# Optimization experiments

Hardware: AMD Instinct MI355X
Metric: run time of the kernel (lower is better)

The kernel has to match this reference:

```python
import jax, jax.numpy as jnp
import numpy as np

B, S, E = 4, 2048, 1024
H, D = 16, 64  # num_heads, head_size; H*D == E


def setup_inputs() -> dict:
    key = jax.random.key(0)
    ks = jax.random.split(key, 6)
    scale = E ** -0.5
    x = jax.random.normal(ks[0], (B, S, E), dtype=jnp.float32)
    # per-head bias-free q/k/v projections, stacked over heads: [H, E, D]
    Wq = jax.random.normal(ks[1], (H, E, D), dtype=jnp.float32) * scale
    Wk = jax.random.normal(ks[2], (H, E, D), dtype=jnp.float32) * scale
    Wv = jax.random.normal(ks[3], (H, E, D), dtype=jnp.float32) * scale
    # output projection: Linear(H*D, E) with bias
    Wproj = jax.random.normal(ks[4], (H * D, E), dtype=jnp.float32) * ((H * D) ** -0.5)
    bproj = jax.random.normal(ks[5], (E,), dtype=jnp.float32) * 0.01
    return {"x": x, "Wq": Wq, "Wk": Wk, "Wv": Wv, "Wproj": Wproj, "bproj": bproj}


def reference(x, Wq, Wk, Wv, Wproj, bproj):
    # Batched equivalent of the per-head loop: each head h computes
    # q = x @ Wq[h], k = x @ Wk[h], v = x @ Wv[h]
    q = jnp.einsum("bse,hed->bhsd", x, Wq)
    k = jnp.einsum("bse,hed->bhsd", x, Wk)
    v = jnp.einsum("bse,hed->bhsd", x, Wv)
    # causal scaled dot-product attention, scale = head_size**-0.5
    scores = jnp.einsum("bhqd,bhkd->bhqk", q, k) * (D ** -0.5)
    causal = jnp.tril(jnp.ones((S, S), dtype=bool))  # [S, S]
    scores = jnp.where(causal, scores, jnp.finfo(scores.dtype).min)
    attn = jax.nn.softmax(scores, axis=-1)  # dropout = identity in eval
    out = jnp.einsum("bhqk,bhkd->bhqd", attn, v)
    # concat heads along the feature dim, then project (dropout = identity)
    out = out.transpose(0, 2, 1, 3).reshape(B, S, H * D)
    return out @ Wproj + bproj
```

## Files before the change

kernel.cpp:

```cpp
#include <hip/hip_runtime.h>
#include <stdint.h>

typedef unsigned short u16;
typedef __attribute__((ext_vector_type(8))) short bf16x8;
typedef __attribute__((ext_vector_type(8))) unsigned short u16x8;
typedef __attribute__((ext_vector_type(4))) float f32x4;

#define S_LEN 2048
#define EDIM 1024
#define NH 16
#define HD 64

static __device__ __forceinline__ u16 f2bf(float f) {
  union { float f; uint32_t u; } v; v.f = f;
  uint32_t r = v.u + 0x7fffu + ((v.u >> 16) & 1u);
  return (u16)(r >> 16);
}

static __device__ __forceinline__ uint32_t cvtpk_bf16(float a, float b) {
  uint32_t r;
  asm("v_cvt_pk_bf16_f32 %0, %1, %2" : "=v"(r) : "v"(a), "v"(b));
  return r;
}

static __device__ __forceinline__ void gload_lds16(const u16* g, u16* l) {
  __builtin_amdgcn_global_load_lds(
      (const __attribute__((address_space(1))) void*)g,
      (__attribute__((address_space(3))) void*)l, 16, 0, 0);
}

static __device__ __forceinline__ bf16x8 gload16(const u16* p) {
  bf16x8 r;
  asm volatile("global_load_dwordx4 %0, %1, off" : "=v"(r) : "v"(p));
  return r;
}

#define WAIT_VM(n)                                   \
  do {                                               \
    asm volatile("s_waitcnt vmcnt(" #n ")");         \
    __builtin_amdgcn_sched_barrier(0);               \
  } while (0)

#define BARRIER()                                    \
  do {                                               \
    __builtin_amdgcn_s_barrier();                    \
    __builtin_amdgcn_sched_barrier(0);               \
  } while (0)

__global__ __launch_bounds__(256) void pack_inputs(
    const float* __restrict__ x, const float* __restrict__ Wq,
    const float* __restrict__ Wk, const float* __restrict__ Wv,
    const float* __restrict__ Wp,
    u16* __restrict__ xb, u16* __restrict__ wqkvT, u16* __restrict__ wprojT) {
  const int blk = blockIdx.x;
  const int tid = threadIdx.x;
  if (blk < 8192) {
    int idx = blk * 256 + tid;
    float4 v = ((const float4*)x)[idx];
    ushort4 o;
    o.x = f2bf(v.x); o.y = f2bf(v.y); o.z = f2bf(v.z); o.w = f2bf(v.w);
    ((ushort4*)xb)[idx] = o;
    return;
  }
  __shared__ u16 tile[64][65];
  const float* src;
  size_t src_rs;
  u16* dst;
  float wscale = 1.0f;
  if (blk < 8960) {
    int t = blk - 8192;
    int mh = t >> 4;
    int et = t & 15;
    int m = mh >> 4, h = mh & 15;
    const float* W = (m == 0) ? Wq : (m == 1) ? Wk : Wv;
    if (m == 0) wscale = 0.1803368801111204f;
    src = W + ((size_t)(h * EDIM + et * 64)) * HD;
    src_rs = HD;
    dst = wqkvT + (size_t)(m * 1024 + h * 64) * 1024 + et * 64;
  } else {
    int t = blk - 8960;
    int kt = t >> 4, nt = t & 15;
    src = Wp + (size_t)(kt * 64) * 1024 + nt * 64;
    src_rs = 1024;
    dst = wprojT + (size_t)(nt * 64) * 1024 + kt * 64;
  }
  {
    const int rr = tid >> 4;
    const int c4 = (tid & 15) << 2;
#pragma unroll
    for (int p = 0; p < 4; p++) {
      const int r = p * 16 + rr;
      float4 v = *(const float4*)(src + (size_t)r * src_rs + c4);
      tile[r][c4 + 0] = f2bf(v.x * wscale);
      tile[r][c4 + 1] = f2bf(v.y * wscale);
      tile[r][c4 + 2] = f2bf(v.z * wscale);
      tile[r][c4 + 3] = f2bf(v.w * wscale);
    }
  }
  __syncthreads();
  {
    const int rr = tid >> 3;
    const int c8 = (tid & 7) << 3;
#pragma unroll
    for (int p = 0; p < 2; p++) {
      const int r = p * 32 + rr;
      u16x8 o;
#pragma unroll
      for (int j = 0; j < 8; j++) o[j] = tile[c8 + j][r];
      *(u16x8*)(dst + (size_t)r * 1024 + c8) = o;
    }
  }
}

template <int EPI>
__global__ __launch_bounds__(256) void gemm128(
    const u16* __restrict__ A, const u16* __restrict__ Bt,
    const float* __restrict__ bias,
    u16* __restrict__ o0, u16* __restrict__ o1, u16* __restrict__ o2,
    float* __restrict__ of, int K, int N) {
  __shared__ __align__(16) u16 As[128 * 64];
  __shared__ __align__(16) u16 Bs[128 * 64];
  const int tid  = threadIdx.x;
  const int lane = tid & 63;
  const int wave = tid >> 6;
  const int wm = wave >> 1;
  const int wn = wave & 1;
  const int col = lane & 15;
  const int quad = lane >> 4;
  const int cs = col & 7;
  const int m0 = blockIdx.y << 7;
  const int n0 = blockIdx.x << 7;

  const int srow  = lane >> 3;
  const int sslot = (lane & 7) ^ srow;
  const u16* gA = A + (size_t)(m0 + (wave << 5) + srow) * K + sslot * 8;
  const u16* gB = Bt + (size_t)(n0 + (wave << 5) + srow) * K + sslot * 8;
  u16* lA = &As[(wave << 5) << 6];
  u16* lB = &Bs[(wave << 5) << 6];

  f32x4 acc[4][4];
#pragma unroll
  for (int i = 0; i < 4; i++)
#pragma unroll
    for (int j = 0; j < 4; j++) acc[i][j] = (f32x4){0.f, 0.f, 0.f, 0.f};

  for (int kk = 0; kk < K; kk += 64) {
    __syncthreads();
#pragma unroll
    for (int i = 0; i < 4; i++) {
      gload_lds16(gA + (size_t)(i * 8) * K + kk, lA + i * 512);
      gload_lds16(gB + (size_t)(i * 8) * K + kk, lB + i * 512);
    }
    __syncthreads();

#pragma unroll
    for (int x = 0; x < 2; x++) {
      bf16x8 af[4], bfr[4];
#pragma unroll
      for (int i = 0; i < 4; i++)
        af[i] = *(const bf16x8*)(
            &As[((wm * 64 + i * 16 + col) << 6) + ((((x << 2) + quad) ^ cs) << 3)]);
#pragma unroll
      for (int j = 0; j < 4; j++)
        bfr[j] = *(const bf16x8*)(
            &Bs[((wn * 64 + j * 16 + col) << 6) + ((((x << 2) + quad) ^ cs) << 3)]);
#pragma unroll
      for (int i = 0; i < 4; i++)
#pragma unroll
        for (int j = 0; j < 4; j++)
          acc[i][j] = __builtin_amdgcn_mfma_f32_16x16x32_bf16(af[i], bfr[j],
                                                              acc[i][j], 0, 0, 0);
    }
  }

#pragma unroll
  for (int i = 0; i < 4; i++) {
#pragma unroll
    for (int j = 0; j < 4; j++) {
      const int rg0 = m0 + wm * 64 + i * 16 + quad * 4;
      const int cg = n0 + wn * 64 + j * 16 + col;
      if (EPI == 0) {
        const int mat = cg >> 10;
        const int rem = cg & 1023;
        const int h = rem >> 6;
        const int d = rem & 63;
        const int b = rg0 >> 11;
        const int s0 = rg0 & 2047;
        if (mat == 2) {
          ushort4 o;
          o.x = f2bf(acc[i][j][0]); o.y = f2bf(acc[i][j][1]);
          o.z = f2bf(acc[i][j][2]); o.w = f2bf(acc[i][j][3]);
          *(ushort4*)(&o2[(((size_t)(b * NH + h) * HD + d) << 11) + s0]) = o;
        } else {
          u16* dst = (mat == 0) ? o0 : o1;
#pragma unroll
          for (int r = 0; r < 4; r++)
            dst[((size_t)((b * NH + h) * S_LEN + s0 + r) << 6) + d] =
                f2bf(acc[i][j][r]);
        }
      } else {
#pragma unroll
        for (int r = 0; r < 4; r++)
          of[(size_t)(rg0 + r) * N + cg] = acc[i][j][r] + bias[cg];
      }
    }
  }
}

__global__ __launch_bounds__(512, 4) void attn_fused(
    const u16* __restrict__ Q, const u16* __restrict__ K,
    const u16* __restrict__ Vt, u16* __restrict__ O) {
  __shared__ __align__(16) u16 Kbuf[2][64 * 64];
  __shared__ __align__(16) u16 Vbuf[2][64 * 64];
  __shared__ __align__(16) u16 Ps[8][16 * 72];

  const int tid  = threadIdx.x;
  const int lane = tid & 63;
  const int wave = tid >> 6;
  const int col  = lane & 15;
  const int quad = lane >> 4;
  const int cs   = col & 7;
  const int gid  = blockIdx.x;
  const int bh = ((gid & 7) << 3) | ((gid >> 3) & 7);
  const int hi = gid >> 6;
  const int qb = (hi < 4) ? (7 - hi) : (hi - 4);
  const int b = bh >> 4;
  const int h = bh & 15;
  const int q0w = qb * 256 + wave * 32;

  const u16* Kbh = K + (size_t)bh * S_LEN * HD;
  const u16* Vbh = Vt + (size_t)bh * HD * S_LEN;

  const int srow  = lane >> 3;
  const int sslot = (lane & 7) ^ srow;
  const int r0 = wave * 8;

  bf16x8 qf[2][2];
#pragma unroll
  for (int a = 0; a < 2; a++) {
    const u16* Qrow = Q + ((size_t)bh * S_LEN + q0w + a * 16 + col) * HD;
    qf[a][0] = gload16(Qrow + quad * 8);
    qf[a][1] = gload16(Qrow + 32 + quad * 8);
  }

  f32x4 oacc[2][4];
#pragma unroll
  for (int a = 0; a < 2; a++)
#pragma unroll
    for (int n = 0; n < 4; n++) oacc[a][n] = (f32x4){0.f, 0.f, 0.f, 0.f};
  float lrow[2][4] = {{0.f, 0.f, 0.f, 0.f}, {0.f, 0.f, 0.f, 0.f}};

  auto STAGE = [&](int buf, int kv0) {
    gload_lds16(Kbh + (size_t)(kv0 + r0 + srow) * HD + sslot * 8,
                &Kbuf[buf][r0 * 64]);
    gload_lds16(Vbh + (size_t)(r0 + srow) * S_LEN + kv0 + sslot * 8,
                &Vbuf[buf][r0 * 64]);
  };

  const int T = 4 * qb + 4;
  int cur = 0;
  STAGE(0, 0);
  WAIT_VM(0);
  BARRIER();

  for (int t = 0; t < T; t++) {
    const int kv0 = t << 6;
    if (t + 1 < T) STAGE(cur ^ 1, kv0 + 64);

    if (kv0 <= q0w + 31) {
      f32x4 sc[2][4];
#pragma unroll
      for (int j = 0; j < 4; j++) {
        const u16* kr = &Kbuf[cur][(j * 16 + col) * 64];
        const bf16x8 kf0 = *(const bf16x8*)(kr + ((quad ^ cs) << 3));
        const bf16x8 kf1 = *(const bf16x8*)(kr + (((4 + quad) ^ cs) << 3));
#pragma unroll
        for (int a = 0; a < 2; a++) {
          sc[a][j] = (f32x4){0.f, 0.f, 0.f, 0.f};
          sc[a][j] = __builtin_amdgcn_mfma_f32_16x16x32_bf16(qf[a][0], kf0, sc[a][j], 0, 0, 0);
          sc[a][j] = __builtin_amdgcn_mfma_f32_16x16x32_bf16(qf[a][1], kf1, sc[a][j], 0, 0, 0);
        }
      }

      const bool diag = (kv0 + 63 > q0w);
#pragma unroll
      for (int a = 0; a < 2; a++) {
#pragma unroll
        for (int r = 0; r < 4; r++) {
          float p[4];
#pragma unroll
          for (int j = 0; j < 4; j++) {
            float v = exp2f(sc[a][j][r]);
            if (diag) {
              const int ql = q0w - kv0 + a * 16 + quad * 4 + r;
              if (j * 16 + col > ql) v = 0.f;
            }
            lrow[a][r] += v;
            p[j] = v;
          }
          const uint32_t pk0 = cvtpk_bf16(p[0], p[1]);
          const uint32_t pk1 = cvtpk_bf16(p[2], p[3]);
          u16* row = &Ps[wave][(quad * 4 + r) * 72 + col];
          row[0]  = (u16)pk0;
          row[16] = (u16)(pk0 >> 16);
          row[32] = (u16)pk1;
          row[48] = (u16)(pk1 >> 16);
        }
        const bf16x8 pf0 = *(const bf16x8*)(&Ps[wave][col * 72 + quad * 8]);
        const bf16x8 pf1 = *(const bf16x8*)(&Ps[wave][col * 72 + 32 + quad * 8]);
#pragma unroll
        for (int n = 0; n < 4; n++) {
          const u16* vr = &Vbuf[cur][(n * 16 + col) * 64];
          const bf16x8 vf0 = *(const bf16x8*)(vr + ((quad ^ cs) << 3));
          const bf16x8 vf1 = *(const bf16x8*)(vr + (((4 + quad) ^ cs) << 3));
          oacc[a][n] = __builtin_amdgcn_mfma_f32_16x16x32_bf16(pf0, vf0, oacc[a][n], 0, 0, 0);
          oacc[a][n] = __builtin_amdgcn_mfma_f32_16x16x32_bf16(pf1, vf1, oacc[a][n], 0, 0, 0);
        }
      }
    }

    WAIT_VM(0);
    BARRIER();
    cur ^= 1;
  }

#pragma unroll
  for (int a = 0; a < 2; a++)
#pragma unroll
    for (int r = 0; r < 4; r++) {
      float l = lrow[a][r];
#pragma unroll
      for (int off = 1; off < 16; off <<= 1) l += __shfl_xor(l, off);
      const float inv = 1.0f / l;
      const size_t row = (size_t)b * S_LEN + q0w + a * 16 + quad * 4 + r;
#pragma unroll
      for (int n = 0; n < 4; n++)
        O[row * EDIM + h * HD + n * 16 + col] = f2bf(oacc[a][n][r] * inv);
    }
}

extern "C" void kernel_launch(void* const* d_in, const int* in_sizes, int n_in,
                              void* d_out, int out_size, void* d_ws, size_t ws_size,
                              hipStream_t stream) {
  const float* x  = (const float*)d_in[0];
  const float* Wq = (const float*)d_in[1];
  const float* Wk = (const float*)d_in[2];
  const float* Wv = (const float*)d_in[3];
  const float* Wp = (const float*)d_in[4];
  const float* bp = (const float*)d_in[5];
  float* out = (float*)d_out;

  char* ws = (char*)d_ws;
  u16* wqkvT  = (u16*)(ws);
  u16* wprojT = (u16*)(ws + 6291456);
  u16* Qb     = (u16*)(ws + 8388608);
  u16* Kb     = (u16*)(ws + 25165824);
  u16* Vtb    = (u16*)(ws + 41943040);
  u16* xb     = (u16*)(ws + 58720256);
  u16* Ob     = xb;

  pack_inputs<<<dim3(9216), dim3(256), 0, stream>>>(x, Wq, Wk, Wv, Wp,
                                                    xb, wqkvT, wprojT);
  gemm128<0><<<dim3(24, 64), dim3(256), 0, stream>>>(
      xb, wqkvT, (const float*)nullptr, Qb, Kb, Vtb, (float*)nullptr, 1024, 3072);
  attn_fused<<<dim3(512), dim3(512), 0, stream>>>(Qb, Kb, Vtb, Ob);
  gemm128<1><<<dim3(8, 64), dim3(256), 0, stream>>>(
      Ob, wprojT, bp, (u16*)nullptr, (u16*)nullptr, (u16*)nullptr, out, 1024, 1024);
}
```

Measured before the change: 275.5 us.

## Halve attention block size to 128 queries and batch P·V loads per V fragment

The attention kernel now uses 256-thread blocks covering 128 query rows, with twice as many blocks (1024), and each wave stages two K/V row groups. Query blocks are now ordered largest-first with a simple descending mapping. The P·V loop is restructured so each V fragment is loaded once and reused for both query sub-tiles, with P stored in per-subtile LDS buffers. This trades more K/V reloads across blocks for finer causal load balancing, less diagonal waste and fewer LDS reads of V.

```diff
diff --git a/kernel.cpp b/kernel.cpp
--- a/kernel.cpp
+++ b/kernel.cpp
@@ -207,12 +207,12 @@
   }
 }
 
-__global__ __launch_bounds__(512, 4) void attn_fused(
+__global__ __launch_bounds__(256, 3) void attn_fused(
     const u16* __restrict__ Q, const u16* __restrict__ K,
     const u16* __restrict__ Vt, u16* __restrict__ O) {
   __shared__ __align__(16) u16 Kbuf[2][64 * 64];
   __shared__ __align__(16) u16 Vbuf[2][64 * 64];
-  __shared__ __align__(16) u16 Ps[8][16 * 72];
+  __shared__ __align__(16) u16 Ps[4][2][16 * 72];
 
   const int tid  = threadIdx.x;
   const int lane = tid & 63;
@@ -222,18 +222,18 @@
   const int cs   = col & 7;
   const int gid  = blockIdx.x;
   const int bh = ((gid & 7) << 3) | ((gid >> 3) & 7);
-  const int hi = gid >> 6;
-  const int qb = (hi < 4) ? (7 - hi) : (hi - 4);
+  const int qb = 15 - (gid >> 6);
   const int b = bh >> 4;
   const int h = bh & 15;
-  const int q0w = qb * 256 + wave * 32;
+  const int q0w = qb * 128 + wave * 32;
 
   const u16* Kbh = K + (size_t)bh * S_LEN * HD;
   const u16* Vbh = Vt + (size_t)bh * HD * S_LEN;
 
   const int srow  = lane >> 3;
   const int sslot = (lane & 7) ^ srow;
-  const int r0 = wave * 8;
+  const int r0a = wave * 16;
+  const int r0b = wave * 16 + 8;
 
   bf16x8 qf[2][2];
 #pragma unroll
@@ -251,13 +251,17 @@
   float lrow[2][4] = {{0.f, 0.f, 0.f, 0.f}, {0.f, 0.f, 0.f, 0.f}};
 
   auto STAGE = [&](int buf, int kv0) {
-    gload_lds16(Kbh + (size_t)(kv0 + r0 + srow) * HD + sslot * 8,
-                &Kbuf[buf][r0 * 64]);
-    gload_lds16(Vbh + (size_t)(r0 + srow) * S_LEN + kv0 + sslot * 8,
-                &Vbuf[buf][r0 * 64]);
+    gload_lds16(Kbh + (size_t)(kv0 + r0a + srow) * HD + sslot * 8,
+                &Kbuf[buf][r0a * 64]);
+    gload_lds16(Kbh + (size_t)(kv0 + r0b + srow) * HD + sslot * 8,
+                &Kbuf[buf][r0b * 64]);
+    gload_lds16(Vbh + (size_t)(r0a + srow) * S_LEN + kv0 + sslot * 8,
+                &Vbuf[buf][r0a * 64]);
+    gload_lds16(Vbh + (size_t)(r0b + srow) * S_LEN + kv0 + sslot * 8,
+                &Vbuf[buf][r0b * 64]);
   };
 
-  const int T = 4 * qb + 4;
+  const int T = 2 * qb + 2;
   int cur = 0;
   STAGE(0, 0);
   WAIT_VM(0);
@@ -284,7 +288,7 @@
 
       const bool diag = (kv0 + 63 > q0w);
 #pragma unroll
-      for (int a = 0; a < 2; a++) {
+      for (int a = 0; a < 2; a++)
 #pragma unroll
         for (int r = 0; r < 4; r++) {
           float p[4];
@@ -300,21 +304,28 @@
           }
           const uint32_t pk0 = cvtpk_bf16(p[0], p[1]);
           const uint32_t pk1 = cvtpk_bf16(p[2], p[3]);
-          u16* row = &Ps[wave][(quad * 4 + r) * 72 + col];
+          u16* row = &Ps[wave][a][(quad * 4 + r) * 72 + col];
           row[0]  = (u16)pk0;
           row[16] = (u16)(pk0 >> 16);
           row[32] = (u16)pk1;
           row[48] = (u16)(pk1 >> 16);
         }
-        const bf16x8 pf0 = *(const bf16x8*)(&Ps[wave][col * 72 + quad * 8]);
-        const bf16x8 pf1 = *(const bf16x8*)(&Ps[wave][col * 72 + 32 + quad * 8]);
-#pragma unroll
-        for (int n = 0; n < 4; n++) {
-          const u16* vr = &Vbuf[cur][(n * 16 + col) * 64];
-          const bf16x8 vf0 = *(const bf16x8*)(vr + ((quad ^ cs) << 3));
-          const bf16x8 vf1 = *(const bf16x8*)(vr + (((4 + quad) ^ cs) << 3));
-          oacc[a][n] = __builtin_amdgcn_mfma_f32_16x16x32_bf16(pf0, vf0, oacc[a][n], 0, 0, 0);
-          oacc[a][n] = __builtin_amdgcn_mfma_f32_16x16x32_bf16(pf1, vf1, oacc[a][n], 0, 0, 0);
+      bf16x8 pf[2][2];
+#pragma unroll
+      for (int a = 0; a < 2; a++) {
+        pf[a][0] = *(const bf16x8*)(&Ps[wave][a][col * 72 + quad * 8]);
+        pf[a][1] = *(const bf16x8*)(&Ps[wave][a][col * 72 + 32 + quad * 8]);
+      }
+
+#pragma unroll
+      for (int n = 0; n < 4; n++) {
+        const u16* vr = &Vbuf[cur][(n * 16 + col) * 64];
+        const bf16x8 vf0 = *(const bf16x8*)(vr + ((quad ^ cs) << 3));
+        const bf16x8 vf1 = *(const bf16x8*)(vr + (((4 + quad) ^ cs) << 3));
+#pragma unroll
+        for (int a = 0; a < 2; a++) {
+          oacc[a][n] = __builtin_amdgcn_mfma_f32_16x16x32_bf16(pf[a][0], vf0, oacc[a][n], 0, 0, 0);
+          oacc[a][n] = __builtin_amdgcn_mfma_f32_16x16x32_bf16(pf[a][1], vf1, oacc[a][n], 0, 0, 0);
         }
       }
     }
@@ -363,7 +374,7 @@
                                                     xb, wqkvT, wprojT);
   gemm128<0><<<dim3(24, 64), dim3(256), 0, stream>>>(
       xb, wqkvT, (const float*)nullptr, Qb, Kb, Vtb, (float*)nullptr, 1024, 3072);
-  attn_fused<<<dim3(512), dim3(512), 0, stream>>>(Qb, Kb, Vtb, Ob);
+  attn_fused<<<dim3(1024), dim3(256), 0, stream>>>(Qb, Kb, Vtb, Ob);
   gemm128<1><<<dim3(8, 64), dim3(256), 0, stream>>>(
       Ob, wprojT, bp, (u16*)nullptr, (u16*)nullptr, (u16*)nullptr, out, 1024, 1024);
 }
```

Measured after the change: 268.2 us. 2.6% less time.
